# Optimization experiments

Hardware: AMD Instinct MI355X
Metric: run time of the kernel (lower is better)

Reference implementation:

```python
import jax, jax.numpy as jnp
import numpy as np

TAU = 2.0        # LIF membrane time constant
VTH = 1.0        # firing threshold
ALPHA = 4.0      # surrogate sigmoid sharpness
BN_EPS = 1e-5

@jax.custom_vjp
def heaviside_surrogate(x):
    # Forward: hard threshold. Backward: sigmoid surrogate gradient (alpha=4).
    return (x >= 0.0).astype(x.dtype)

def _hs_fwd(x):
    return heaviside_surrogate(x), x

def _hs_bwd(x, g):
    s = jax.nn.sigmoid(ALPHA * x)
    return (g * ALPHA * s * (1.0 - s),)

heaviside_surrogate.defvjp(_hs_fwd, _hs_bwd)


def setup_inputs() -> dict:
    key = jax.random.key(0)
    k1, k2 = jax.random.split(key)
    B, Cin, T, Cout = 64, 512, 1024, 256
    x = jax.random.normal(k1, (B, Cin, T), dtype=jnp.float32)
    W = jax.random.normal(k2, (Cout, Cin), dtype=jnp.float32) * (1.0 / np.sqrt(Cin))
    gamma = jnp.ones((Cout,), dtype=jnp.float32)
    beta = jnp.zeros((Cout,), dtype=jnp.float32)
    run_mean = jnp.zeros((Cout,), dtype=jnp.float32)
    run_var = jnp.ones((Cout,), dtype=jnp.float32)
    return {"x": x, "W": W, "gamma": gamma, "beta": beta,
            "run_mean": run_mean, "run_var": run_var}


def reference(x, W, gamma, beta, run_mean, run_var):
    # Dropout is identity in eval mode.
    # conv1d, kernel_size=1, no bias -> pointwise GEMM over channels: [B,Cin,T] -> [B,Cout,T]
    y = jnp.einsum('bct,oc->bot', x, W)
    # BatchNorm1d (inference, running stats), per-channel affine
    inv = jax.lax.rsqrt(run_var + BN_EPS)
    y = (y - run_mean[None, :, None]) * (inv * gamma)[None, :, None] + beta[None, :, None]
    # LIF recurrence over the time dim (last axis), hard reset to 0, detach_reset.
    yt = jnp.transpose(y, (2, 0, 1))  # [T, B, Cout]

    def step(v, x_t):
        v = v + (x_t - v) / TAU              # decay_input charge
        s = heaviside_surrogate(v - VTH)     # spike via surrogate threshold
        v = v * (1.0 - jax.lax.stop_gradient(s))  # hard reset (detached)
        return v, s

    v0 = jnp.zeros(yt.shape[1:], dtype=yt.dtype)
    _, spikes = jax.lax.scan(step, v0, yt)   # spikes: [T, B, Cout]
    # out.mean(dim=-1) == spike rate over time
    return spikes.mean(axis=0)               # [B, Cout]
```

## Files before the change

### kernel.cpp

```cpp
#include <hip/hip_runtime.h>
#include <math.h>

typedef _Float16 f16;
typedef __attribute__((ext_vector_type(8)))  _Float16 f16v8;
typedef __attribute__((ext_vector_type(2)))  __fp16   h16v2;
typedef __attribute__((ext_vector_type(16))) float    f32x16;
typedef __attribute__((ext_vector_type(4)))  float    f32x4;

namespace {
constexpr int kB = 64, kCin = 512, kT = 1024, kCout = 256;
constexpr size_t kYBytes     = (size_t)kB * kT * kCout * 4;
constexpr size_t kWfragBytes = (size_t)32 * 8 * 2 * 64 * 16;
constexpr size_t kSBytes     = kCout * 4;
constexpr size_t kWsNeed     = kYBytes + kWfragBytes + kSBytes;
}

__global__ void wsplit16_kernel(const float* __restrict__ W, const float* __restrict__ gamma,
                                const float* __restrict__ rvar,
                                f16* __restrict__ wfrag, float* __restrict__ sarr) {
    const int kc = blockIdx.x, osub = blockIdx.y, p = blockIdx.z;
    const int lane = threadIdx.x;
    const int o  = osub * 32 + (lane & 31);
    const int kb = kc * 16 + (lane >> 5) * 8;
    f16v8 frag;
#pragma unroll
    for (int j = 0; j < 8; ++j) {
        const float w = 32.0f * W[o * kCin + kb + j];
        const f16 h = (f16)w;
        const float r = w - (float)h;
        const f16 l = (f16)(r * 2048.0f);
        frag[j] = p ? l : h;
    }
    *reinterpret_cast<f16v8*>(wfrag + ((size_t)((kc * 8 + osub) * 2 + p) * 64 + lane) * 8) = frag;
    if (kc == 0 && osub == 0 && p == 0) {
#pragma unroll
        for (int j = 0; j < 4; ++j) {
            const int oo = j * 64 + lane;
            sarr[oo] = (float)((double)gamma[oo] / sqrt((double)rvar[oo] + 1e-5));
        }
    }
}

__global__ __launch_bounds__(512, 4)
void gemm_f16_kernel(const float* __restrict__ x, const f16* __restrict__ wfrag,
                     const float* __restrict__ sarr, const float* __restrict__ rmean,
                     const float* __restrict__ beta, float* __restrict__ yt) {
    __shared__ unsigned int Bd[4][64 * 20];

    const int tid  = threadIdx.x;
    const int lane = tid & 63;
    const int wave = tid >> 6;
    const int n = lane & 31, q = lane >> 5;
    const int b   = blockIdx.y;
    const int tg0 = blockIdx.x * 64;
    const int osg = wave;
    const float* __restrict__ xb = x + ((size_t)b << 19);
    const f16v8* __restrict__ wf = reinterpret_cast<const f16v8*>(wfrag);

    const int st_t = lane;
    const int kpp  = wave;
    const int st_sw = (st_t >> 3) & 3;
    const int wr_base = 20 * st_t;
    const int dw0 = (((kpp >> 2) + 0) ^ st_sw) * 4 + (kpp & 3);
    const int dw1 = (((kpp >> 2) + 2) ^ st_sw) * 4 + (kpp & 3);

    f32x16 accA[2] = {};
    f32x16 accB[2] = {};
    f16v8  af[2][2];
    float  xq[4][2];

    auto loadX = [&](int kc, float (&xd)[2]) {
        const float* px = xb + (size_t)(kc * 16 + 2 * kpp) * kT + tg0 + st_t;
        xd[0] = px[0];
        xd[1] = px[kT];
    };
    auto loadA = [&](int kc, f16v8 (&ad)[2]) {
#pragma unroll
        for (int p = 0; p < 2; ++p)
            ad[p] = wf[(size_t)((kc * 8 + osg) * 2 + p) * 64 + lane];
    };
    auto stage = [&](int buf, const float (&xd)[2]) {
        auto h01 = __builtin_amdgcn_cvt_pkrtz(xd[0], xd[1]);
        auto l01 = __builtin_amdgcn_cvt_pkrtz((xd[0] - (float)h01[0]) * 2048.0f,
                                              (xd[1] - (float)h01[1]) * 2048.0f);
        *reinterpret_cast<h16v2*>(&Bd[buf][wr_base + dw0]) = h01;
        *reinterpret_cast<h16v2*>(&Bd[buf][wr_base + dw1]) = l01;
    };
    auto domfma = [&](int buf, const f16v8 (&ad)[2]) {
        __builtin_amdgcn_s_setprio(1);
#pragma unroll
        for (int s = 0; s < 2; ++s) {
            const int t = s * 32 + n;
            const int sw = (t >> 3) & 3;
            const f16v8 bh = *reinterpret_cast<const f16v8*>(&Bd[buf][20 * t + 4 * ((0 + q) ^ sw)]);
            const f16v8 bl = *reinterpret_cast<const f16v8*>(&Bd[buf][20 * t + 4 * ((2 + q) ^ sw)]);
            accA[s] = __builtin_amdgcn_mfma_f32_32x32x16_f16(ad[0], bh, accA[s], 0, 0, 0);
            accB[s] = __builtin_amdgcn_mfma_f32_32x32x16_f16(ad[0], bl, accB[s], 0, 0, 0);
            accB[s] = __builtin_amdgcn_mfma_f32_32x32x16_f16(ad[1], bh, accB[s], 0, 0, 0);
        }
        __builtin_amdgcn_s_setprio(0);
    };

    loadX(0, xq[0]); loadX(1, xq[1]); loadX(2, xq[2]); loadX(3, xq[3]);
    loadA(0, af[0]);
    stage(0, xq[0]);
    stage(1, xq[1]);
    asm volatile("s_waitcnt lgkmcnt(0)\n\ts_barrier" ::: "memory");

    for (int kc4 = 0; kc4 < 8; ++kc4) {
#pragma unroll
        for (int u = 0; u < 4; ++u) {
            const int kc = kc4 * 4 + u;
            if (kc < 31) loadA(kc + 1, af[(u + 1) & 1]);
            if (kc < 30) stage((u + 2) & 3, xq[(u + 2) & 3]);
            if (kc < 28) loadX(kc + 4, xq[u]);
            domfma(u, af[u & 1]);
            if (u & 1)
                asm volatile("s_waitcnt lgkmcnt(0)\n\ts_barrier" ::: "memory");
        }
    }

#pragma unroll
    for (int s = 0; s < 2; ++s) {
        const f32x16 v = accA[s] + accB[s] * 4.8828125e-4f;
        const size_t t = (size_t)tg0 + s * 32 + n;
#pragma unroll
        for (int g = 0; g < 4; ++g) {
            const int og = osg * 32 + g * 8 + q * 4;
            const f32x4 sv = *reinterpret_cast<const f32x4*>(sarr + og);
            const f32x4 mv = *reinterpret_cast<const f32x4*>(rmean + og);
            const f32x4 bv = *reinterpret_cast<const f32x4*>(beta + og);
#pragma unroll
            for (int r2 = 0; r2 < 4; ++r2) {
                const int o = og + r2;
                const float val = (v[4 * g + r2] * 0.03125f - mv[r2]) * sv[r2] + bv[r2];
                yt[(((size_t)b << 8) + (size_t)o) * 1024 + t] = val;
            }
        }
    }
}

__global__ __launch_bounds__(64)
void lif_kernel(const float* __restrict__ yt, float* __restrict__ out) {
    const int b = blockIdx.x >> 2;
    const int o = ((blockIdx.x & 3) << 6) + threadIdx.x;
    const f32x4* __restrict__ row =
        reinterpret_cast<const f32x4*>(yt) + (((size_t)b << 8) + (size_t)o) * 256;
    float v = 0.f;
    int cnt = 0;
    f32x4 qb[16];
#pragma unroll
    for (int u = 0; u < 16; ++u) qb[u] = row[u];
    for (int jj = 0; jj < 15; ++jj) {
#pragma unroll
        for (int u = 0; u < 16; ++u) {
            const f32x4 cv = qb[u];
            qb[u] = row[jj * 16 + u + 16];
#pragma unroll
            for (int e = 0; e < 4; ++e) {
                v = v + (cv[e] - v) * 0.5f;
                if (v - 1.0f >= 0.0f) { ++cnt; v = 0.f; }
            }
        }
    }
#pragma unroll
    for (int u = 0; u < 16; ++u) {
        const f32x4 cv = qb[u];
#pragma unroll
        for (int e = 0; e < 4; ++e) {
            v = v + (cv[e] - v) * 0.5f;
            if (v - 1.0f >= 0.0f) { ++cnt; v = 0.f; }
        }
    }
    out[((size_t)b << 8) + o] = (float)cnt * (1.0f / 1024.0f);
}

namespace fb {
constexpr int kOTile = 32, kTTile = 128, kCc = 64;
constexpr int kNtt = kT / kTTile, kNcc = kCin / kCc, kYPad = 132;
}

__global__ void wt_transpose_kernel(const float* __restrict__ W, float* __restrict__ Wt) {
    int idx = blockIdx.x * 256 + threadIdx.x;
    int c = idx >> 8, o = idx & 255;
    Wt[idx] = W[o * kCin + c];
}

__global__ __launch_bounds__(256, 2)
void snn_fused_kernel(const float* __restrict__ x, const float* __restrict__ Wt,
                      const float* __restrict__ gamma, const float* __restrict__ beta,
                      const float* __restrict__ rmean, const float* __restrict__ rvar,
                      float* __restrict__ out) {
    using namespace fb;
    __shared__ float xs[kCc][kTTile];
    __shared__ float ws[kCc][kOTile];
    __shared__ float ytile[kOTile][kYPad];
    __shared__ float sarr[kOTile], barr[kOTile], marr[kOTile], vstate[kOTile];
    __shared__ int scnt[kOTile];
    const int tid = threadIdx.x, tx = tid & 31, ty = tid >> 5;
    const int b = blockIdx.y, o_blk = blockIdx.x * kOTile;
    if (tid < kOTile) {
        const int o = o_blk + tid;
        const double dinv = 1.0 / sqrt((double)rvar[o] + 1e-5);
        sarr[tid] = (float)(dinv * (double)gamma[o]);
        barr[tid] = beta[o]; marr[tid] = rmean[o];
        vstate[tid] = 0.0f; scnt[tid] = 0;
    }
    __syncthreads();
    const float* xb = x + (size_t)b * kCin * kT;
    for (int tt = 0; tt < kNtt; ++tt) {
        float acc[4][4];
#pragma unroll
        for (int i = 0; i < 4; ++i)
#pragma unroll
            for (int j = 0; j < 4; ++j) acc[i][j] = 0.0f;
        const int t0 = tt * kTTile;
        for (int cc = 0; cc < kNcc; ++cc) {
#pragma unroll
            for (int k = 0; k < 8; ++k) {
                const int f = tid + 256 * k;
                const int c = f >> 5, tq = f & 31;
                *reinterpret_cast<float4*>(&xs[c][tq * 4]) = *reinterpret_cast<const float4*>(
                    xb + (size_t)(cc * kCc + c) * kT + t0 + tq * 4);
            }
#pragma unroll
            for (int k = 0; k < 2; ++k) {
                const int f = tid + 256 * k;
                const int c = f >> 3, oq = f & 7;
                *reinterpret_cast<float4*>(&ws[c][oq * 4]) = *reinterpret_cast<const float4*>(
                    Wt + (size_t)(cc * kCc + c) * kCout + o_blk + oq * 4);
            }
            __syncthreads();
#pragma unroll 8
            for (int c = 0; c < kCc; ++c) {
                const float4 xv = *reinterpret_cast<const float4*>(&xs[c][tx * 4]);
                const float4 wv = *reinterpret_cast<const float4*>(&ws[c][ty * 4]);
                const float xf[4] = {xv.x, xv.y, xv.z, xv.w};
                const float wf4[4] = {wv.x, wv.y, wv.z, wv.w};
#pragma unroll
                for (int i = 0; i < 4; ++i)
#pragma unroll
                    for (int j = 0; j < 4; ++j) acc[i][j] += wf4[i] * xf[j];
            }
            __syncthreads();
        }
#pragma unroll
        for (int i = 0; i < 4; ++i) {
            const int o = ty * 4 + i;
            const float s = sarr[o], bb2 = barr[o], m = marr[o];
#pragma unroll
            for (int j = 0; j < 4; ++j) ytile[o][tx * 4 + j] = (acc[i][j] - m) * s + bb2;
        }
        __syncthreads();
        if (tid < kOTile) {
            float vv = vstate[tid];
            int cnt = 0;
#pragma unroll 4
            for (int t = 0; t < kTTile; ++t) {
                const float yv = ytile[tid][t];
                vv = vv + (yv - vv) * 0.5f;
                if (vv - 1.0f >= 0.0f) { cnt++; vv = 0.0f; }
            }
            vstate[tid] = vv; scnt[tid] += cnt;
        }
        __syncthreads();
    }
    if (tid < kOTile) out[b * kCout + o_blk + tid] = (float)scnt[tid] * (1.0f / 1024.0f);
}

extern "C" void kernel_launch(void* const* d_in, const int* in_sizes, int n_in,
                              void* d_out, int out_size, void* d_ws, size_t ws_size,
                              hipStream_t stream) {
    const float* x     = (const float*)d_in[0];
    const float* W     = (const float*)d_in[1];
    const float* gamma = (const float*)d_in[2];
    const float* beta  = (const float*)d_in[3];
    const float* rmean = (const float*)d_in[4];
    const float* rvar  = (const float*)d_in[5];
    float* out = (float*)d_out;

    if (ws_size >= kWsNeed) {
        float* yt    = (float*)d_ws;
        f16*   wfrag = (f16*)((char*)d_ws + kYBytes);
        float* sarr  = (float*)((char*)d_ws + kYBytes + kWfragBytes);
        wsplit16_kernel<<<dim3(32, 8, 2), 64, 0, stream>>>(W, gamma, rvar, wfrag, sarr);
        gemm_f16_kernel<<<dim3(16, 64), 512, 0, stream>>>(x, wfrag, sarr, rmean, beta, yt);
        lif_kernel<<<256, 64, 0, stream>>>(yt, out);
    } else {
        float* Wt = (float*)d_ws;
        wt_transpose_kernel<<<(kCin * kCout) / 256, 256, 0, stream>>>(W, Wt);
        snn_fused_kernel<<<dim3(kCout / fb::kOTile, kB), 256, 0, stream>>>(
            x, Wt, gamma, beta, rmean, rvar, out);
    }
}
```

Baseline: 258.7 us.

## Load x fragments directly into registers, drop LDS staging and barriers

```diff
diff --git a/kernel.cpp b/kernel.cpp
--- a/kernel.cpp
+++ b/kernel.cpp
@@ -3,7 +3,6 @@
 
 typedef _Float16 f16;
 typedef __attribute__((ext_vector_type(8)))  _Float16 f16v8;
-typedef __attribute__((ext_vector_type(2)))  __fp16   h16v2;
 typedef __attribute__((ext_vector_type(16))) float    f32x16;
 typedef __attribute__((ext_vector_type(4)))  float    f32x4;
 
@@ -41,82 +40,78 @@
     }
 }
 
-__global__ __launch_bounds__(512, 4)
+__global__ __launch_bounds__(256, 3)
 void gemm_f16_kernel(const float* __restrict__ x, const f16* __restrict__ wfrag,
                      const float* __restrict__ sarr, const float* __restrict__ rmean,
                      const float* __restrict__ beta, float* __restrict__ yt) {
-    __shared__ unsigned int Bd[4][64 * 20];
-
     const int tid  = threadIdx.x;
     const int lane = tid & 63;
     const int wave = tid >> 6;
     const int n = lane & 31, q = lane >> 5;
     const int b   = blockIdx.y;
-    const int tg0 = blockIdx.x * 64;
-    const int osg = wave;
+    const int tg0 = (blockIdx.x >> 1) * 64;
+    const int osg = (blockIdx.x & 1) * 4 + wave;
     const float* __restrict__ xb = x + ((size_t)b << 19);
     const f16v8* __restrict__ wf = reinterpret_cast<const f16v8*>(wfrag);
 
-    const int st_t = lane;
-    const int kpp  = wave;
-    const int st_sw = (st_t >> 3) & 3;
-    const int wr_base = 20 * st_t;
-    const int dw0 = (((kpp >> 2) + 0) ^ st_sw) * 4 + (kpp & 3);
-    const int dw1 = (((kpp >> 2) + 2) ^ st_sw) * 4 + (kpp & 3);
+    const float* __restrict__ xp0 = xb + (size_t)(q * 8) * kT + tg0 + n;
+    const float* __restrict__ xp1 = xp0 + 32;
 
     f32x16 accA[2] = {};
     f32x16 accB[2] = {};
     f16v8  af[2][2];
-    float  xq[4][2];
-
-    auto loadX = [&](int kc, float (&xd)[2]) {
-        const float* px = xb + (size_t)(kc * 16 + 2 * kpp) * kT + tg0 + st_t;
-        xd[0] = px[0];
-        xd[1] = px[kT];
+    float  xr[2][2][8];
+
+    auto loadX = [&](int kc, float (&xd)[2][8]) {
+        const float* p0 = xp0 + (size_t)kc * 16 * kT;
+        const float* p1 = xp1 + (size_t)kc * 16 * kT;
+#pragma unroll
+        for (int j = 0; j < 8; ++j) {
+            xd[0][j] = p0[(size_t)j * kT];
+            xd[1][j] = p1[(size_t)j * kT];
+        }
     };
     auto loadA = [&](int kc, f16v8 (&ad)[2]) {
 #pragma unroll
         for (int p = 0; p < 2; ++p)
             ad[p] = wf[(size_t)((kc * 8 + osg) * 2 + p) * 64 + lane];
     };
-    auto stage = [&](int buf, const float (&xd)[2]) {
-        auto h01 = __builtin_amdgcn_cvt_pkrtz(xd[0], xd[1]);
-        auto l01 = __builtin_amdgcn_cvt_pkrtz((xd[0] - (float)h01[0]) * 2048.0f,
-                                              (xd[1] - (float)h01[1]) * 2048.0f);
-        *reinterpret_cast<h16v2*>(&Bd[buf][wr_base + dw0]) = h01;
-        *reinterpret_cast<h16v2*>(&Bd[buf][wr_base + dw1]) = l01;
-    };
-    auto domfma = [&](int buf, const f16v8 (&ad)[2]) {
+    auto convert = [&](const float (&xd)[2][8], f16v8 (&bh)[2], f16v8 (&bl)[2]) {
+#pragma unroll
+        for (int s = 0; s < 2; ++s)
+#pragma unroll
+            for (int jj = 0; jj < 4; ++jj) {
+                auto h = __builtin_amdgcn_cvt_pkrtz(xd[s][2 * jj], xd[s][2 * jj + 1]);
+                auto l = __builtin_amdgcn_cvt_pkrtz((xd[s][2 * jj]     - (float)h[0]) * 2048.0f,
+                                                    (xd[s][2 * jj + 1] - (float)h[1]) * 2048.0f);
+                bh[s][2 * jj] = h[0]; bh[s][2 * jj + 1] = h[1];
+                bl[s][2 * jj] = l[0]; bl[s][2 * jj + 1] = l[1];
+            }
+    };
+    auto domfma = [&](const f16v8 (&ad)[2], const f16v8 (&bh)[2], const f16v8 (&bl)[2]) {
         __builtin_amdgcn_s_setprio(1);
 #pragma unroll
         for (int s = 0; s < 2; ++s) {
-            const int t = s * 32 + n;
-            const int sw = (t >> 3) & 3;
-            const f16v8 bh = *reinterpret_cast<const f16v8*>(&Bd[buf][20 * t + 4 * ((0 + q) ^ sw)]);
-            const f16v8 bl = *reinterpret_cast<const f16v8*>(&Bd[buf][20 * t + 4 * ((2 + q) ^ sw)]);
-            accA[s] = __builtin_amdgcn_mfma_f32_32x32x16_f16(ad[0], bh, accA[s], 0, 0, 0);
-            accB[s] = __builtin_amdgcn_mfma_f32_32x32x16_f16(ad[0], bl, accB[s], 0, 0, 0);
-            accB[s] = __builtin_amdgcn_mfma_f32_32x32x16_f16(ad[1], bh, accB[s], 0, 0, 0);
+            accA[s] = __builtin_amdgcn_mfma_f32_32x32x16_f16(ad[0], bh[s], accA[s], 0, 0, 0);
+            accB[s] = __builtin_amdgcn_mfma_f32_32x32x16_f16(ad[0], bl[s], accB[s], 0, 0, 0);
+            accB[s] = __builtin_amdgcn_mfma_f32_32x32x16_f16(ad[1], bh[s], accB[s], 0, 0, 0);
         }
         __builtin_amdgcn_s_setprio(0);
     };
 
-    loadX(0, xq[0]); loadX(1, xq[1]); loadX(2, xq[2]); loadX(3, xq[3]);
+    loadX(0, xr[0]);
     loadA(0, af[0]);
-    stage(0, xq[0]);
-    stage(1, xq[1]);
-    asm volatile("s_waitcnt lgkmcnt(0)\n\ts_barrier" ::: "memory");
-
-    for (int kc4 = 0; kc4 < 8; ++kc4) {
-#pragma unroll
-        for (int u = 0; u < 4; ++u) {
-            const int kc = kc4 * 4 + u;
-            if (kc < 31) loadA(kc + 1, af[(u + 1) & 1]);
-            if (kc < 30) stage((u + 2) & 3, xq[(u + 2) & 3]);
-            if (kc < 28) loadX(kc + 4, xq[u]);
-            domfma(u, af[u & 1]);
-            if (u & 1)
-                asm volatile("s_waitcnt lgkmcnt(0)\n\ts_barrier" ::: "memory");
+    for (int kc2 = 0; kc2 < 16; ++kc2) {
+#pragma unroll
+        for (int u = 0; u < 2; ++u) {
+            const int kc = kc2 * 2 + u;
+            if (kc < 31) {
+                loadX(kc + 1, xr[(u + 1) & 1]);
+                loadA(kc + 1, af[(u + 1) & 1]);
+            }
+            f16v8 bh[2], bl[2];
+            convert(xr[u & 1], bh, bl);
+            domfma(af[u & 1], bh, bl);
         }
     }
 
@@ -284,7 +279,7 @@
         f16*   wfrag = (f16*)((char*)d_ws + kYBytes);
         float* sarr  = (float*)((char*)d_ws + kYBytes + kWfragBytes);
         wsplit16_kernel<<<dim3(32, 8, 2), 64, 0, stream>>>(W, gamma, rvar, wfrag, sarr);
-        gemm_f16_kernel<<<dim3(16, 64), 512, 0, stream>>>(x, wfrag, sarr, rmean, beta, yt);
+        gemm_f16_kernel<<<dim3(32, 64), 256, 0, stream>>>(x, wfrag, sarr, rmean, beta, yt);
         lif_kernel<<<256, 64, 0, stream>>>(yt, out);
     } else {
         float* Wt = (float*)d_ws;
```

Result: slower. 306.9 us (+18.6%).
